# Kernel tuning notes

Measured on AMD Instinct MI355X. Metric: run time of the kernel, lower is better.

The kernel has to match this reference:

```python
import jax, jax.numpy as jnp
import numpy as np

INPUT_SIZE = 2048
HIDDEN_SIZE = 2048
BATCH = 4096
COMBINED = INPUT_SIZE + HIDDEN_SIZE


def setup_inputs() -> dict:
    key = jax.random.key(0)
    ks = jax.random.split(key, 11)
    s = 1.0 / np.sqrt(COMBINED)  # torch Linear default init scale
    inp = {
        "x_t": jax.random.normal(ks[0], (BATCH, INPUT_SIZE), jnp.float32),
        "h_prev": jax.random.normal(ks[1], (BATCH, HIDDEN_SIZE), jnp.float32),
        "c_prev": jax.random.normal(ks[2], (BATCH, HIDDEN_SIZE), jnp.float32),
        # torch nn.Linear weights: [out, in]
        "W_f": jax.random.uniform(ks[3], (HIDDEN_SIZE, COMBINED), jnp.float32, -s, s),
        "b_f": jax.random.uniform(ks[4], (HIDDEN_SIZE,), jnp.float32, -s, s),
        "W_i": jax.random.uniform(ks[5], (HIDDEN_SIZE, COMBINED), jnp.float32, -s, s),
        "b_i": jax.random.uniform(ks[6], (HIDDEN_SIZE,), jnp.float32, -s, s),
        "W_c": jax.random.uniform(ks[7], (HIDDEN_SIZE, COMBINED), jnp.float32, -s, s),
        "b_c": jax.random.uniform(ks[8], (HIDDEN_SIZE,), jnp.float32, -s, s),
        "W_o": jax.random.uniform(ks[9], (HIDDEN_SIZE, COMBINED), jnp.float32, -s, s),
        "b_o": jax.random.uniform(ks[10], (HIDDEN_SIZE,), jnp.float32, -s, s),
    }
    return inp


def reference(x_t, h_prev, c_prev, W_f, b_f, W_i, b_i, W_c, b_c, W_o, b_o):
    # combined = cat([h_prev, x_t], dim=1)  -> [B, H + I]
    combined = jnp.concatenate([h_prev, x_t], axis=1)
    # Fuse the four gate GEMMs into one [B, C] x [C, 4H] matmul.
    W = jnp.concatenate([W_f, W_i, W_c, W_o], axis=0)  # [4H, C]
    b = jnp.concatenate([b_f, b_i, b_c, b_o], axis=0)  # [4H]
    gates = combined @ W.T + b  # [B, 4H]
    gf, gi, gc, go = jnp.split(gates, 4, axis=1)
    f_t = jax.nn.sigmoid(gf)
    i_t = jax.nn.sigmoid(gi)
    c_tilde = jnp.tanh(gc)
    o_t = jax.nn.sigmoid(go)
    c_t = f_t * c_prev + i_t * c_tilde
    h_t = o_t * jnp.tanh(c_t)
    return (h_t, c_t)
```

## Files before the change

### kernel.cpp

```cpp
#include <hip/hip_runtime.h>
#include <hip/hip_bf16.h>
#include <cstdint>

#define B_DIM 4096
#define H_DIM 2048
#define I_DIM 2048
#define K_DIM 4096
#define N4    8192

typedef unsigned int u32;
typedef unsigned short u16;
typedef __attribute__((ext_vector_type(4))) float floatx4;
typedef __attribute__((ext_vector_type(8))) short bf16x8;
typedef __attribute__((ext_vector_type(8))) float f32x8;
typedef __attribute__((ext_vector_type(8))) __bf16 bfx8;

__device__ static inline void gload16(const void* g, void* l) {
    __builtin_amdgcn_global_load_lds(
        (const __attribute__((address_space(1))) u32*)g,
        (__attribute__((address_space(3))) u32*)l, 16, 0, 0);
}
__device__ static inline float fast_sig(float x) {
    return 1.f / (1.f + __expf(-x));
}
__device__ static inline float fast_tanh(float x) {
    float ax = fabsf(x);
    float t = __expf(-2.f * ax);
    float r = (1.f - t) / (1.f + t);
    return copysignf(r, x);
}

__global__ void convert_all(const float* __restrict__ h_prev, const float* __restrict__ x_t,
                            const float* __restrict__ Wf, const float* __restrict__ Wi,
                            const float* __restrict__ Wc, const float* __restrict__ Wo,
                            u16* __restrict__ comb, u16* __restrict__ wb) {
    const int bid = blockIdx.x;
    const float* src;
    u16* dst;
    if (bid < 8192) {
        int base = (bid * 256 + (int)threadIdx.x) * 8;
        int row = base >> 12, col = base & 4095;
        src = (col < H_DIM) ? h_prev + (size_t)row * H_DIM + col
                            : x_t    + (size_t)row * I_DIM + (col - H_DIM);
        dst = comb + base;
    } else {
        long long base = ((long long)(bid - 8192) * 256 + threadIdx.x) * 8;
        int n = (int)(base >> 12), col = (int)(base & 4095);
        int row128 = n & 127;
        int g = (row128 >> 4) & 3;
        int j = (n >> 7) * 32 + ((row128 >> 6) << 4) + (row128 & 15);
        const float* W = (g == 0) ? Wf : (g == 1) ? Wi : (g == 2) ? Wc : Wo;
        src = W + (size_t)j * K_DIM + col;
        dst = wb + base;
    }
    float4 v0 = *(const float4*)src;
    float4 v1 = *(const float4*)(src + 4);
    f32x8 f = { v0.x, v0.y, v0.z, v0.w, v1.x, v1.y, v1.z, v1.w };
    *(bfx8*)dst = __builtin_convertvector(f, bfx8);
}

#define TILE(T, VMS, DOSTAGE)                                                   \
  {                                                                             \
    asm volatile("s_waitcnt vmcnt(" VMS ")" ::: "memory");                      \
    __builtin_amdgcn_s_barrier();                                               \
    __builtin_amdgcn_sched_barrier(0);                                          \
    const u16* sA_ = lsA[(T) & 3];                                              \
    const u16* sB_ = lsB[(T) & 3];                                              \
    if (DOSTAGE) {                                                              \
      const u16* as_ = aSrc + ((T) + 3) * 32;                                   \
      char* dA_ = (char*)lsA[((T) + 3) & 3] + doff;                             \
      gload16(as_, dA_);                                                        \
      gload16(as_ + 128 * K_DIM, dA_ + 8192);                                   \
    }                                                                           \
    bf16x8 afL_[4], afH_[4], bb_[4];                                            \
    _Pragma("unroll") for (int i_ = 0; i_ < 4; ++i_)                            \
      afL_[i_] = *(const bf16x8*)&sA_[(wm2 + i_ * 16 + r) * 32 + qsw];          \
    _Pragma("unroll") for (int g_ = 0; g_ < 4; ++g_)                            \
      bb_[g_] = *(const bf16x8*)&sB_[(wn2 + g_ * 16 + r) * 32 + qsw];           \
    __builtin_amdgcn_s_setprio(1);                                              \
    _Pragma("unroll") for (int i_ = 0; i_ < 4; ++i_)                            \
      _Pragma("unroll") for (int g_ = 0; g_ < 4; ++g_)                          \
        acc[i_][g_] = __builtin_amdgcn_mfma_f32_16x16x32_bf16(                  \
            afL_[i_], bb_[g_], acc[i_][g_], 0, 0, 0);                           \
    __builtin_amdgcn_s_setprio(0);                                              \
    _Pragma("unroll") for (int i_ = 0; i_ < 4; ++i_)                            \
      afH_[i_] = *(const bf16x8*)&sA_[(wm2 + 64 + i_ * 16 + r) * 32 + qsw];     \
    if (DOSTAGE) {                                                              \
      const u16* bs_ = bSrc + ((T) + 3) * 32;                                   \
      char* dB_ = (char*)lsB[((T) + 3) & 3] + doff;                             \
      gload16(bs_, dB_);                                                        \
      gload16(bs_ + 128 * K_DIM, dB_ + 8192);                                   \
    }                                                                           \
    __builtin_amdgcn_s_barrier();                                               \
    __builtin_amdgcn_sched_barrier(0);                                          \
    __builtin_amdgcn_s_setprio(1);                                              \
    _Pragma("unroll") for (int i_ = 0; i_ < 4; ++i_)                            \
      _Pragma("unroll") for (int g_ = 0; g_ < 4; ++g_)                          \
        acc[4 + i_][g_] = __builtin_amdgcn_mfma_f32_16x16x32_bf16(              \
            afH_[i_], bb_[g_], acc[4 + i_][g_], 0, 0, 0);                       \
    __builtin_amdgcn_s_setprio(0);                                              \
  }

__global__ __launch_bounds__(512, 2) void gemm_lstm(const u16* __restrict__ A,
                                                    const u16* __restrict__ Bm,
                                                    const float* __restrict__ c_prev,
                                                    const float* __restrict__ bf_,
                                                    const float* __restrict__ bi_,
                                                    const float* __restrict__ bc_,
                                                    const float* __restrict__ bo_,
                                                    float* __restrict__ out) {
    __shared__ __align__(16) u16 lsA[4][256 * 32];
    __shared__ __align__(16) u16 lsB[4][256 * 32];

    const int tid  = threadIdx.x;
    const int lane = tid & 63;
    const int wave = tid >> 6;
    const int wm2  = (wave >> 2) * 128;
    const int wn2  = (wave & 3) * 64;
    const int quad = lane >> 4;
    const int r    = lane & 15;
    const int qsw  = (quad ^ ((r >> 1) & 3)) * 8;
    const int mb   = blockIdx.y * 256;
    const int nbT  = blockIdx.x * 256;

    const int ko = ((tid & 3) ^ ((tid >> 3) & 3)) * 8;
    const u16* aSrc = A  + (size_t)(mb  + (tid >> 2)) * K_DIM + ko;
    const u16* bSrc = Bm + (size_t)(nbT + (tid >> 2)) * K_DIM + ko;
    const int doff = tid * 16;

    floatx4 acc[8][4];
#pragma unroll
    for (int i = 0; i < 8; ++i)
#pragma unroll
        for (int g = 0; g < 4; ++g)
            acc[i][g] = (floatx4){0.f, 0.f, 0.f, 0.f};

#pragma unroll
    for (int pt = 0; pt < 3; ++pt) {
        const u16* as_ = aSrc + pt * 32;
        char* dA_ = (char*)lsA[pt] + doff;
        gload16(as_, dA_);
        gload16(as_ + 128 * K_DIM, dA_ + 8192);
        const u16* bs_ = bSrc + pt * 32;
        char* dB_ = (char*)lsB[pt] + doff;
        gload16(bs_, dB_);
        gload16(bs_ + 128 * K_DIM, dB_ + 8192);
    }

#pragma unroll 1
    for (int t = 0; t < 125; ++t) TILE(t, "8", 1);
    TILE(125, "8", 0);
    TILE(126, "0", 0);
    TILE(127, "0", 0);

    __builtin_amdgcn_sched_barrier(0);

    const int j = blockIdx.x * 64 + (wave & 3) * 16 + r;
    const float bfv = bf_[j], biv = bi_[j], bcv = bc_[j], bov = bo_[j];
    const int rowb = mb + wm2 + quad * 4;
    const float* cp = c_prev + (size_t)rowb * H_DIM + j;
    float* oh = out + (size_t)rowb * H_DIM + j;
    float* oc = oh + (size_t)B_DIM * H_DIM;
#pragma unroll
    for (int i = 0; i < 8; ++i) {
#pragma unroll
        for (int rg = 0; rg < 4; ++rg) {
            size_t off = (size_t)(i * 16 + rg) * H_DIM;
            float gf = acc[i][0][rg] + bfv;
            float gi = acc[i][1][rg] + biv;
            float gc = acc[i][2][rg] + bcv;
            float go = acc[i][3][rg] + bov;
            float f  = fast_sig(gf);
            float ii = fast_sig(gi);
            float ct = fast_tanh(gc);
            float oo = fast_sig(go);
            float c  = f * cp[off] + ii * ct;
            float h  = oo * fast_tanh(c);
            oh[off] = h;
            oc[off] = c;
        }
    }
}

__global__ void lstm_naive(const float* __restrict__ x_t, const float* __restrict__ h_prev,
                           const float* __restrict__ c_prev,
                           const float* __restrict__ Wf, const float* __restrict__ bf_,
                           const float* __restrict__ Wi, const float* __restrict__ bi_,
                           const float* __restrict__ Wc, const float* __restrict__ bc_,
                           const float* __restrict__ Wo, const float* __restrict__ bo_,
                           float* __restrict__ out) {
    int j = blockIdx.x * blockDim.x + threadIdx.x;
    int b = blockIdx.y;
    const float* hrow = h_prev + (long long)b * H_DIM;
    const float* xrow = x_t   + (long long)b * I_DIM;
    const float* wf = Wf + (long long)j * K_DIM;
    const float* wi = Wi + (long long)j * K_DIM;
    const float* wc = Wc + (long long)j * K_DIM;
    const float* wo = Wo + (long long)j * K_DIM;
    float af = bf_[j], ai = bi_[j], ac = bc_[j], ao = bo_[j];
    for (int k = 0; k < H_DIM; k += 4) {
        float4 v = *(const float4*)(hrow + k);
        float4 a = *(const float4*)(wf + k);
        float4 bqi = *(const float4*)(wi + k);
        float4 cq = *(const float4*)(wc + k);
        float4 dq = *(const float4*)(wo + k);
        af += v.x*a.x + v.y*a.y + v.z*a.z + v.w*a.w;
        ai += v.x*bqi.x + v.y*bqi.y + v.z*bqi.z + v.w*bqi.w;
        ac += v.x*cq.x + v.y*cq.y + v.z*cq.z + v.w*cq.w;
        ao += v.x*dq.x + v.y*dq.y + v.z*dq.z + v.w*dq.w;
    }
    for (int k = 0; k < I_DIM; k += 4) {
        float4 v = *(const float4*)(xrow + k);
        float4 a = *(const float4*)(wf + H_DIM + k);
        float4 bqi = *(const float4*)(wi + H_DIM + k);
        float4 cq = *(const float4*)(wc + H_DIM + k);
        float4 dq = *(const float4*)(wo + H_DIM + k);
        af += v.x*a.x + v.y*a.y + v.z*a.z + v.w*a.w;
        ai += v.x*bqi.x + v.y*bqi.y + v.z*bqi.z + v.w*bqi.w;
        ac += v.x*cq.x + v.y*cq.y + v.z*cq.z + v.w*cq.w;
        ao += v.x*dq.x + v.y*dq.y + v.z*dq.z + v.w*dq.w;
    }
    float f  = 1.f / (1.f + __expf(-af));
    float ii = 1.f / (1.f + __expf(-ai));
    float ct = tanhf(ac);
    float oo = 1.f / (1.f + __expf(-ao));
    int t = b * H_DIM + j;
    float c = f * c_prev[t] + ii * ct;
    out[t] = oo * tanhf(c);
    out[B_DIM * H_DIM + t] = c;
}

extern "C" void kernel_launch(void* const* d_in, const int* in_sizes, int n_in,
                              void* d_out, int out_size, void* d_ws, size_t ws_size,
                              hipStream_t stream) {
    const float* x_t    = (const float*)d_in[0];
    const float* h_prev = (const float*)d_in[1];
    const float* c_prev = (const float*)d_in[2];
    const float* Wf = (const float*)d_in[3];  const float* bf_ = (const float*)d_in[4];
    const float* Wi = (const float*)d_in[5];  const float* bi_ = (const float*)d_in[6];
    const float* Wc = (const float*)d_in[7];  const float* bc_ = (const float*)d_in[8];
    const float* Wo = (const float*)d_in[9];  const float* bo_ = (const float*)d_in[10];
    float* out = (float*)d_out;

    const size_t comb_elems = (size_t)B_DIM * K_DIM;
    const size_t wb_elems   = (size_t)N4 * K_DIM;
    const size_t need = (comb_elems + wb_elems) * sizeof(u16);

    if (ws_size >= need) {
        u16* comb = (u16*)d_ws;
        u16* wb   = comb + comb_elems;
        convert_all<<<24576, 256, 0, stream>>>(h_prev, x_t, Wf, Wi, Wc, Wo, comb, wb);
        dim3 grid(N4 / 256, B_DIM / 256);
        gemm_lstm<<<grid, 512, 0, stream>>>(comb, wb, c_prev, bf_, bi_, bc_, bo_, out);
    } else {
        dim3 grid(H_DIM / 256, B_DIM);
        lstm_naive<<<grid, 256, 0, stream>>>(x_t, h_prev, c_prev,
                                             Wf, bf_, Wi, bi_, Wc, bc_, Wo, bo_, out);
    }
}
```

Before: 547.4 us.

## Use 1024-thread blocks with 16 waves each owning a 64x64 sub-tile

The GEMM block grows from 8 to 16 waves while keeping the 256x256 tile. Each wave now computes a 64x64 output piece instead of 128x64, which halves the accumulator registers per thread and removes the second barrier and MFMA phase inside each k-step. Each thread issues one async LDS load per operand per stage, and the vmcnt waits are adjusted to match. The aim is more waves in flight to hide latency. In exchange, each wave does less MFMA work per LDS fragment it loads, and the 128 KB of LDS per block may prevent running several blocks per CU as the launch bounds ask.

```diff
diff --git a/kernel.cpp b/kernel.cpp
--- a/kernel.cpp
+++ b/kernel.cpp
@@ -64,59 +64,41 @@
     asm volatile("s_waitcnt vmcnt(" VMS ")" ::: "memory");                      \
     __builtin_amdgcn_s_barrier();                                               \
     __builtin_amdgcn_sched_barrier(0);                                          \
+    if (DOSTAGE) {                                                              \
+      gload16(aSrc + ((T) + 3) * 32, (char*)lsA[((T) + 3) & 3] + doff);         \
+      gload16(bSrc + ((T) + 3) * 32, (char*)lsB[((T) + 3) & 3] + doff);         \
+    }                                                                           \
     const u16* sA_ = lsA[(T) & 3];                                              \
     const u16* sB_ = lsB[(T) & 3];                                              \
-    if (DOSTAGE) {                                                              \
-      const u16* as_ = aSrc + ((T) + 3) * 32;                                   \
-      char* dA_ = (char*)lsA[((T) + 3) & 3] + doff;                             \
-      gload16(as_, dA_);                                                        \
-      gload16(as_ + 128 * K_DIM, dA_ + 8192);                                   \
-    }                                                                           \
-    bf16x8 afL_[4], afH_[4], bb_[4];                                            \
+    bf16x8 af_[4], bb_[4];                                                      \
     _Pragma("unroll") for (int i_ = 0; i_ < 4; ++i_)                            \
-      afL_[i_] = *(const bf16x8*)&sA_[(wm2 + i_ * 16 + r) * 32 + qsw];          \
+      af_[i_] = *(const bf16x8*)&sA_[(wm3 + i_ * 16 + r) * 32 + qsw];           \
     _Pragma("unroll") for (int g_ = 0; g_ < 4; ++g_)                            \
-      bb_[g_] = *(const bf16x8*)&sB_[(wn2 + g_ * 16 + r) * 32 + qsw];           \
+      bb_[g_] = *(const bf16x8*)&sB_[(wn3 + g_ * 16 + r) * 32 + qsw];           \
     __builtin_amdgcn_s_setprio(1);                                              \
     _Pragma("unroll") for (int i_ = 0; i_ < 4; ++i_)                            \
       _Pragma("unroll") for (int g_ = 0; g_ < 4; ++g_)                          \
         acc[i_][g_] = __builtin_amdgcn_mfma_f32_16x16x32_bf16(                  \
-            afL_[i_], bb_[g_], acc[i_][g_], 0, 0, 0);                           \
-    __builtin_amdgcn_s_setprio(0);                                              \
-    _Pragma("unroll") for (int i_ = 0; i_ < 4; ++i_)                            \
-      afH_[i_] = *(const bf16x8*)&sA_[(wm2 + 64 + i_ * 16 + r) * 32 + qsw];     \
-    if (DOSTAGE) {                                                              \
-      const u16* bs_ = bSrc + ((T) + 3) * 32;                                   \
-      char* dB_ = (char*)lsB[((T) + 3) & 3] + doff;                             \
-      gload16(bs_, dB_);                                                        \
-      gload16(bs_ + 128 * K_DIM, dB_ + 8192);                                   \
-    }                                                                           \
-    __builtin_amdgcn_s_barrier();                                               \
-    __builtin_amdgcn_sched_barrier(0);                                          \
-    __builtin_amdgcn_s_setprio(1);                                              \
-    _Pragma("unroll") for (int i_ = 0; i_ < 4; ++i_)                            \
-      _Pragma("unroll") for (int g_ = 0; g_ < 4; ++g_)                          \
-        acc[4 + i_][g_] = __builtin_amdgcn_mfma_f32_16x16x32_bf16(              \
-            afH_[i_], bb_[g_], acc[4 + i_][g_], 0, 0, 0);                       \
+            af_[i_], bb_[g_], acc[i_][g_], 0, 0, 0);                            \
     __builtin_amdgcn_s_setprio(0);                                              \
   }
 
-__global__ __launch_bounds__(512, 2) void gemm_lstm(const u16* __restrict__ A,
-                                                    const u16* __restrict__ Bm,
-                                                    const float* __restrict__ c_prev,
-                                                    const float* __restrict__ bf_,
-                                                    const float* __restrict__ bi_,
-                                                    const float* __restrict__ bc_,
-                                                    const float* __restrict__ bo_,
-                                                    float* __restrict__ out) {
+__global__ __launch_bounds__(1024, 4) void gemm_lstm(const u16* __restrict__ A,
+                                                     const u16* __restrict__ Bm,
+                                                     const float* __restrict__ c_prev,
+                                                     const float* __restrict__ bf_,
+                                                     const float* __restrict__ bi_,
+                                                     const float* __restrict__ bc_,
+                                                     const float* __restrict__ bo_,
+                                                     float* __restrict__ out) {
     __shared__ __align__(16) u16 lsA[4][256 * 32];
     __shared__ __align__(16) u16 lsB[4][256 * 32];
 
     const int tid  = threadIdx.x;
     const int lane = tid & 63;
     const int wave = tid >> 6;
-    const int wm2  = (wave >> 2) * 128;
-    const int wn2  = (wave & 3) * 64;
+    const int wm3  = (wave >> 2) * 64;
+    const int wn3  = (wave & 3) * 64;
     const int quad = lane >> 4;
     const int r    = lane & 15;
     const int qsw  = (quad ^ ((r >> 1) & 3)) * 8;
@@ -128,41 +110,35 @@
     const u16* bSrc = Bm + (size_t)(nbT + (tid >> 2)) * K_DIM + ko;
     const int doff = tid * 16;
 
-    floatx4 acc[8][4];
-#pragma unroll
-    for (int i = 0; i < 8; ++i)
+    floatx4 acc[4][4];
+#pragma unroll
+    for (int i = 0; i < 4; ++i)
 #pragma unroll
         for (int g = 0; g < 4; ++g)
             acc[i][g] = (floatx4){0.f, 0.f, 0.f, 0.f};
 
 #pragma unroll
     for (int pt = 0; pt < 3; ++pt) {
-        const u16* as_ = aSrc + pt * 32;
-        char* dA_ = (char*)lsA[pt] + doff;
-        gload16(as_, dA_);
-        gload16(as_ + 128 * K_DIM, dA_ + 8192);
-        const u16* bs_ = bSrc + pt * 32;
-        char* dB_ = (char*)lsB[pt] + doff;
-        gload16(bs_, dB_);
-        gload16(bs_ + 128 * K_DIM, dB_ + 8192);
+        gload16(aSrc + pt * 32, (char*)lsA[pt] + doff);
+        gload16(bSrc + pt * 32, (char*)lsB[pt] + doff);
     }
 
 #pragma unroll 1
-    for (int t = 0; t < 125; ++t) TILE(t, "8", 1);
-    TILE(125, "8", 0);
-    TILE(126, "0", 0);
+    for (int t = 0; t < 125; ++t) TILE(t, "4", 1);
+    TILE(125, "4", 0);
+    TILE(126, "2", 0);
     TILE(127, "0", 0);
 
     __builtin_amdgcn_sched_barrier(0);
 
     const int j = blockIdx.x * 64 + (wave & 3) * 16 + r;
     const float bfv = bf_[j], biv = bi_[j], bcv = bc_[j], bov = bo_[j];
-    const int rowb = mb + wm2 + quad * 4;
+    const int rowb = mb + wm3 + quad * 4;
     const float* cp = c_prev + (size_t)rowb * H_DIM + j;
     float* oh = out + (size_t)rowb * H_DIM + j;
     float* oc = oh + (size_t)B_DIM * H_DIM;
 #pragma unroll
-    for (int i = 0; i < 8; ++i) {
+    for (int i = 0; i < 4; ++i) {
 #pragma unroll
         for (int rg = 0; rg < 4; ++rg) {
             size_t off = (size_t)(i * 16 + rg) * H_DIM;
@@ -251,7 +227,7 @@
         u16* wb   = comb + comb_elems;
         convert_all<<<24576, 256, 0, stream>>>(h_prev, x_t, Wf, Wi, Wc, Wo, comb, wb);
         dim3 grid(N4 / 256, B_DIM / 256);
-        gemm_lstm<<<grid, 512, 0, stream>>>(comb, wb, c_prev, bf_, bi_, bc_, bo_, out);
+        gemm_lstm<<<grid, 1024, 0, stream>>>(comb, wb, c_prev, bf_, bi_, bc_, bo_, out);
     } else {
         dim3 grid(H_DIM / 256, B_DIM);
         lstm_naive<<<grid, 256, 0, stream>>>(x_t, h_prev, c_prev,
```

Measured after the change: 548.2 us. Within noise of the previous version (+0.2%).
